# Optimization experiments

Hardware: AMD Instinct MI355X
Metric: run time of the kernel (lower is better)

Reference implementation:

```python
import jax, jax.numpy as jnp
import numpy as np

B, H, S, D = 4, 8, 2048, 64
NEG = -1e9


def setup_inputs() -> dict:
    key = jax.random.key(0)
    k1, k2, k3, k4 = jax.random.split(key, 4)
    qs = jax.random.normal(k1, (B, H, S, D), dtype=jnp.float32)
    ks = jax.random.normal(k2, (B, H, S, D), dtype=jnp.float32)
    vs = jax.random.normal(k3, (B, H, S, D), dtype=jnp.float32)
    # binary 0/1 float mask, broadcast over heads
    mask = (jax.random.uniform(k4, (B, 1, S, S)) < 0.5).astype(jnp.float32)
    return {"qs": qs, "ks": ks, "vs": vs, "mask": mask}


def reference(qs, ks, vs, mask):
    scale = 1.0 / np.sqrt(qs.shape[-1]).astype(np.float32)
    # [B,H,S,S] logits; multiplicative pre-mask, then additive -1e9 on masked slots
    logits = jnp.einsum('bhqd,bhkd->bhqk', qs, ks) * mask * scale
    logits = logits + (1.0 - mask) * NEG
    weights = jax.nn.softmax(logits, axis=-1) * mask  # multiplicative post-mask
    return jnp.einsum('bhqk,bhkd->bhqd', weights, vs)
```

## Files before the change

### kernel.cpp

```cpp
#include <hip/hip_runtime.h>
#include <stdint.h>

#define S_LEN 2048
#define NTILE 32

typedef float f32x4 __attribute__((ext_vector_type(4)));
typedef short bf16x8 __attribute__((ext_vector_type(8)));

__device__ __forceinline__ uint16_t f2bf(float f) {
    uint32_t u = __float_as_uint(f);
    return (uint16_t)((u + 0x7FFFu + ((u >> 16) & 1u)) >> 16);
}

#define SWZ(r, cb) (((r) << 7) + ((cb) ^ (((r) & 7) << 4)))

#define AS3PTR(p) ((__attribute__((address_space(3))) uint32_t*)(uintptr_t)(p))
#define AS1PTR(p) ((const __attribute__((address_space(1))) uint32_t*)(uintptr_t)(p))

__global__ __launch_bounds__(256)
void prep_all(const float* __restrict__ K, const float* __restrict__ V,
              const float* __restrict__ M, uint8_t* __restrict__ Kswz,
              uint8_t* __restrict__ Vtswz, unsigned long long* __restrict__ Mb)
{
    const int bid = blockIdx.x;
    const int tid = threadIdx.x;
    if (bid < 2048) {
        int flat = bid * 256 + tid;
        int cb = flat & 7, r = (flat >> 3) & 63, kt = (flat >> 9) & 31, bh = flat >> 14;
        const float* src = K + (((size_t)bh * S_LEN + kt * 64 + r) << 6) + cb * 8;
        f32x4 a = *(const f32x4*)src;
        f32x4 b = *(const f32x4*)(src + 4);
        bf16x8 o;
        o[0] = (short)f2bf(a[0]); o[1] = (short)f2bf(a[1]);
        o[2] = (short)f2bf(a[2]); o[3] = (short)f2bf(a[3]);
        o[4] = (short)f2bf(b[0]); o[5] = (short)f2bf(b[1]);
        o[6] = (short)f2bf(b[2]); o[7] = (short)f2bf(b[3]);
        *(bf16x8*)(Kswz + (((size_t)(bh * 32 + kt)) << 13) + SWZ(r, cb * 16)) = o;
    } else if (bid < 4096) {
        int flat = (bid - 2048) * 256 + tid;
        int d = flat & 63, ck = (flat >> 6) & 7, kt = (flat >> 9) & 31, bh = flat >> 14;
        const float* src = V + (((size_t)bh * S_LEN + kt * 64 + ck * 8) << 6) + d;
        bf16x8 o;
        #pragma unroll
        for (int i = 0; i < 8; ++i) o[i] = (short)f2bf(src[i << 6]);
        *(bf16x8*)(Vtswz + (((size_t)(bh * 32 + kt)) << 13) + SWZ(d, ck * 16)) = o;
    } else {
        int wave = (bid - 4096) * 4 + (tid >> 6);
        int lane = tid & 63;
        size_t w0 = (size_t)wave * 16;
        for (int i = 0; i < 16; ++i) {
            size_t widx = w0 + i;
            float m = M[(widx << 6) + lane];
            unsigned long long bits = __ballot(m > 0.5f);
            if (lane == 0) Mb[widx] = bits;
        }
    }
}

#define K_OFF 0
#define V_OFF 16384

__global__ __launch_bounds__(256, 4)
void attn_fwd(const float* __restrict__ Q, const uint8_t* __restrict__ Kswz,
              const uint8_t* __restrict__ Vtswz,
              const unsigned long long* __restrict__ Mb,
              float* __restrict__ O)
{
    __shared__ __align__(16) uint8_t lds[32768];

    const int tid  = threadIdx.x;
    const int lane = tid & 63;
    const int w    = tid >> 6;
    const int g    = lane >> 4;
    const int c    = lane & 15;

    const int bid0 = blockIdx.x;
    const int bid  = ((bid0 & 7) << 7) + (bid0 >> 3);
    const int bh  = bid >> 5;
    const int qt  = bid & 31;
    const int b   = bh >> 3;
    const int q0  = qt << 6;

    const float QSCL = 0.125f * 1.44269504088896340736f;
    bf16x8 qf[2];
    {
        const float* qrow = Q + (((size_t)bh * S_LEN + q0 + w * 16 + c) << 6);
        #pragma unroll
        for (int kb = 0; kb < 2; ++kb) {
            f32x4 a  = *(const f32x4*)(qrow + kb * 32 + g * 8);
            f32x4 b4 = *(const f32x4*)(qrow + kb * 32 + g * 8 + 4);
            bf16x8 f;
            f[0] = (short)f2bf(a[0] * QSCL);  f[1] = (short)f2bf(a[1] * QSCL);
            f[2] = (short)f2bf(a[2] * QSCL);  f[3] = (short)f2bf(a[3] * QSCL);
            f[4] = (short)f2bf(b4[0] * QSCL); f[5] = (short)f2bf(b4[1] * QSCL);
            f[6] = (short)f2bf(b4[2] * QSCL); f[7] = (short)f2bf(b4[3] * QSCL);
            qf[kb] = f;
        }
    }

    f32x4 acc[4];
    #pragma unroll
    for (int dt = 0; dt < 4; ++dt) acc[dt] = (f32x4){0.f, 0.f, 0.f, 0.f};
    float lsum = 0.f;

    const unsigned long long* mrow =
        Mb + ((size_t)(b * S_LEN + q0 + w * 16 + c) << 5);

    const uint8_t* kbh = Kswz  + ((size_t)(bh * 32) << 13);
    const uint8_t* vbh = Vtswz + ((size_t)(bh * 32) << 13);

    auto stage = [&](int buf, int t) {
        #pragma unroll
        for (int it = 0; it < 2; ++it) {
            int off = ((w << 1) + it) << 10;
            __builtin_amdgcn_global_load_lds(
                AS1PTR(kbh + ((size_t)t << 13) + off + lane * 16),
                AS3PTR(&lds[K_OFF + (buf << 13) + off]), 16, 0, 0);
            __builtin_amdgcn_global_load_lds(
                AS1PTR(vbh + ((size_t)t << 13) + off + lane * 16),
                AS3PTR(&lds[V_OFF + (buf << 13) + off]), 16, 0, 0);
        }
    };

    stage(0, 0);
    __syncthreads();

    #pragma unroll 2
    for (int kt = 0; kt < NTILE; ++kt) {
        const int buf = kt & 1;
        if (kt + 1 < NTILE) stage(buf ^ 1, kt + 1);

        unsigned long long mw = mrow[kt];

        const uint8_t* kb = &lds[K_OFF + (buf << 13)];
        f32x4 sacc[4];
        #pragma unroll
        for (int ct = 0; ct < 4; ++ct) {
            bf16x8 kf0 = *(const bf16x8*)(kb + SWZ(16 * ct + c, 16 * g));
            bf16x8 kf1 = *(const bf16x8*)(kb + SWZ(16 * ct + c, 64 + 16 * g));
            f32x4 z = (f32x4){0.f, 0.f, 0.f, 0.f};
            z = __builtin_amdgcn_mfma_f32_16x16x32_bf16(kf0, qf[0], z, 0, 0, 0);
            z = __builtin_amdgcn_mfma_f32_16x16x32_bf16(kf1, qf[1], z, 0, 0, 0);
            sacc[ct] = z;
        }

        uint32_t pd[4][2];
        unsigned long long msh = mw >> (4 * g);
        uint32_t ulo = (uint32_t)msh, uhi = (uint32_t)(msh >> 32);
        #pragma unroll
        for (int ct = 0; ct < 4; ++ct) {
            uint32_t sel = (ct & 2) ? uhi : ulo;
            float e[4];
            #pragma unroll
            for (int j = 0; j < 4; ++j) {
                float x = sacc[ct][j];
                x = (sel & (1u << (16 * (ct & 1) + j))) ? x : -1000.f;
                asm("v_exp_f32 %0, %1" : "=v"(e[j]) : "v"(x));
                lsum += e[j];
            }
            asm("v_cvt_pk_bf16_f32 %0, %1, %2" : "=v"(pd[ct][0]) : "v"(e[0]), "v"(e[1]));
            asm("v_cvt_pk_bf16_f32 %0, %1, %2" : "=v"(pd[ct][1]) : "v"(e[2]), "v"(e[3]));
        }

        const uint8_t* vb = &lds[V_OFF + (buf << 13)];
        #pragma unroll
        for (int kp = 0; kp < 2; ++kp) {
            uint32_t a0 = pd[2 * kp][0], b0 = pd[2 * kp + 1][0];
            uint32_t a1 = pd[2 * kp][1], b1 = pd[2 * kp + 1][1];
            asm("v_permlane32_swap_b32 %0, %1" : "+v"(a0), "+v"(b0));
            asm("v_permlane16_swap_b32 %0, %1" : "+v"(a0), "+v"(b0));
            asm("v_permlane32_swap_b32 %0, %1" : "+v"(a1), "+v"(b1));
            asm("v_permlane16_swap_b32 %0, %1" : "+v"(a1), "+v"(b1));
            union { uint32_t d[4]; bf16x8 v; } pu;
            pu.d[0] = a0; pu.d[1] = a1; pu.d[2] = b0; pu.d[3] = b1;
            #pragma unroll
            for (int dt = 0; dt < 4; ++dt) {
                bf16x8 vf = *(const bf16x8*)(vb + SWZ(c + 16 * dt, kp * 64 + 16 * g));
                acc[dt] = __builtin_amdgcn_mfma_f32_16x16x32_bf16(pu.v, vf, acc[dt], 0, 0, 0);
            }
        }

        __syncthreads();
    }

    float l = lsum;
    l += __shfl_xor(l, 16, 64);
    l += __shfl_xor(l, 32, 64);
    float linv = (l > 0.f) ? 1.f / l : 0.f;
    float inv[4];
    #pragma unroll
    for (int j = 0; j < 4; ++j) inv[j] = __shfl(linv, 4 * g + j, 64);

    float* obase = O + (((size_t)bh * S_LEN + q0 + w * 16) << 6);
    #pragma unroll
    for (int j = 0; j < 4; ++j)
        #pragma unroll
        for (int dt = 0; dt < 4; ++dt)
            obase[((4 * g + j) << 6) + c + 16 * dt] = acc[dt][j] * inv[j];
}

extern "C" void kernel_launch(void* const* d_in, const int* in_sizes, int n_in,
                              void* d_out, int out_size, void* d_ws, size_t ws_size,
                              hipStream_t stream) {
    const float* qs   = (const float*)d_in[0];
    const float* ks   = (const float*)d_in[1];
    const float* vs   = (const float*)d_in[2];
    const float* mask = (const float*)d_in[3];
    float* out = (float*)d_out;
    (void)in_sizes; (void)n_in; (void)out_size; (void)ws_size;

    uint8_t* ws = (uint8_t*)d_ws;
    uint8_t* Kswz  = ws;
    uint8_t* Vtswz = ws + (8u << 20);
    unsigned long long* Mb = (unsigned long long*)(ws + (16u << 20));

    hipLaunchKernelGGL(prep_all, dim3(8192), dim3(256), 0, stream,
                       ks, vs, mask, Kswz, Vtswz, Mb);
    hipLaunchKernelGGL(attn_fwd, dim3(1024), dim3(256), 0, stream,
                       qs, Kswz, Vtswz, Mb, out);
}
```

Baseline: 81.33 us.

## Split key tiles across waves with register-resident fragments and LDS reduction

Restructures attention so each wave handles all 64 query rows for a quarter of every key tile, loading K/V fragments straight from global memory into registers in MFMA-ready layouts instead of staging through shared memory with barriers. The prep kernel now writes K and V in per-lane fragment order and packs the mask into 16-bit words per lane via an LDS transpose. Partial outputs and row sums are combined across the four waves through LDS at the end. This removes per-tile barriers and LDS traffic, at the cost of more registers (occupancy hint lowered to 3), a cross-wave reduction, and a larger mask-prep phase.

```diff
diff --git a/kernel.cpp b/kernel.cpp
--- a/kernel.cpp
+++ b/kernel.cpp
@@ -6,22 +6,31 @@
 
 typedef float f32x4 __attribute__((ext_vector_type(4)));
 typedef short bf16x8 __attribute__((ext_vector_type(8)));
+typedef short s16x4 __attribute__((ext_vector_type(4)));
 
 __device__ __forceinline__ uint16_t f2bf(float f) {
     uint32_t u = __float_as_uint(f);
     return (uint16_t)((u + 0x7FFFu + ((u >> 16) & 1u)) >> 16);
 }
 
-#define SWZ(r, cb) (((r) << 7) + ((cb) ^ (((r) & 7) << 4)))
-
-#define AS3PTR(p) ((__attribute__((address_space(3))) uint32_t*)(uintptr_t)(p))
-#define AS1PTR(p) ((const __attribute__((address_space(1))) uint32_t*)(uintptr_t)(p))
+#if __has_builtin(__builtin_amdgcn_mfma_f32_16x16x16bf16_1k)
+__device__ __forceinline__ f32x4 mfma16(s16x4 a, s16x4 b, f32x4 c) {
+    return __builtin_amdgcn_mfma_f32_16x16x16bf16_1k(a, b, c, 0, 0, 0);
+}
+#else
+__device__ __forceinline__ f32x4 mfma16(s16x4 a, s16x4 b, f32x4 c) {
+    bf16x8 az = {a[0], a[1], a[2], a[3], 0, 0, 0, 0};
+    bf16x8 bz = {b[0], b[1], b[2], b[3], 0, 0, 0, 0};
+    return __builtin_amdgcn_mfma_f32_16x16x32_bf16(az, bz, c, 0, 0, 0);
+}
+#endif
 
 __global__ __launch_bounds__(256)
 void prep_all(const float* __restrict__ K, const float* __restrict__ V,
-              const float* __restrict__ M, uint8_t* __restrict__ Kswz,
-              uint8_t* __restrict__ Vtswz, unsigned long long* __restrict__ Mb)
+              const float* __restrict__ M, uint8_t* __restrict__ Kd,
+              uint8_t* __restrict__ Vd, uint16_t* __restrict__ Mp)
 {
+    __shared__ float mt[4096];
     const int bid = blockIdx.x;
     const int tid = threadIdx.x;
     if (bid < 2048) {
@@ -35,38 +44,48 @@
         o[2] = (short)f2bf(a[2]); o[3] = (short)f2bf(a[3]);
         o[4] = (short)f2bf(b[0]); o[5] = (short)f2bf(b[1]);
         o[6] = (short)f2bf(b[2]); o[7] = (short)f2bf(b[3]);
-        *(bf16x8*)(Kswz + (((size_t)(bh * 32 + kt)) << 13) + SWZ(r, cb * 16)) = o;
-    } else if (bid < 4096) {
-        int flat = (bid - 2048) * 256 + tid;
-        int d = flat & 63, ck = (flat >> 6) & 7, kt = (flat >> 9) & 31, bh = flat >> 14;
-        const float* src = V + (((size_t)bh * S_LEN + kt * 64 + ck * 8) << 6) + d;
-        bf16x8 o;
-        #pragma unroll
-        for (int i = 0; i < 8; ++i) o[i] = (short)f2bf(src[i << 6]);
-        *(bf16x8*)(Vtswz + (((size_t)(bh * 32 + kt)) << 13) + SWZ(d, ck * 16)) = o;
+        size_t chunk = ((((size_t)(bh * 32 + kt) * 4 + (r >> 4)) * 2 + (cb >> 2)) << 6)
+                       + ((cb & 3) << 4) + (r & 15);
+        *(bf16x8*)(Kd + chunk * 16) = o;
+    } else if (bid < 6144) {
+        int vf = (bid - 2048) * 256 + tid;
+        int c = vf & 15, g = (vf >> 4) & 3, dt = (vf >> 6) & 3;
+        int w = (vf >> 8) & 3, kt = (vf >> 10) & 31, bh = vf >> 15;
+        const float* src = V + (((size_t)bh * S_LEN + kt * 64 + 16 * w + 4 * g) << 6)
+                           + 16 * dt + c;
+        s16x4 o;
+        #pragma unroll
+        for (int j = 0; j < 4; ++j) o[j] = (short)f2bf(src[j << 6]);
+        size_t chunk = (((size_t)(bh * 32 + kt) * 16 + w * 4 + dt) << 6) + g * 16 + c;
+        *(s16x4*)(Vd + chunk * 8) = o;
     } else {
-        int wave = (bid - 4096) * 4 + (tid >> 6);
-        int lane = tid & 63;
-        size_t w0 = (size_t)wave * 16;
-        for (int i = 0; i < 16; ++i) {
-            size_t widx = w0 + i;
-            float m = M[(widx << 6) + lane];
-            unsigned long long bits = __ballot(m > 0.5f);
-            if (lane == 0) Mb[widx] = bits;
-        }
-    }
-}
-
-#define K_OFF 0
-#define V_OFF 16384
-
-__global__ __launch_bounds__(256, 4)
-void attn_fwd(const float* __restrict__ Q, const uint8_t* __restrict__ Kswz,
-              const uint8_t* __restrict__ Vtswz,
-              const unsigned long long* __restrict__ Mb,
+        int mid = bid - 6144;
+        int b = mid >> 10, qt = (mid >> 5) & 31, kt = mid & 31;
+        int row = tid >> 2, cc = tid & 3;
+        const float* src = M + ((size_t)(b * S_LEN + qt * 64 + row) * S_LEN) + kt * 64;
+        #pragma unroll
+        for (int i = 0; i < 4; ++i)
+            *(f32x4*)&mt[(row << 6) + cc * 16 + i * 4] =
+                *(const f32x4*)(src + cc * 16 + i * 4);
+        __syncthreads();
+        int l = tid & 63, w = tid >> 6, g = l >> 4, c = l & 15;
+        uint32_t m = 0;
+        #pragma unroll
+        for (int qc = 0; qc < 4; ++qc)
+            #pragma unroll
+            for (int j = 0; j < 4; ++j)
+                m |= (mt[((16 * qc + c) << 6) + 16 * w + 4 * g + j] > 0.5f)
+                     << (qc * 4 + j);
+        Mp[(size_t)mid * 256 + tid] = (uint16_t)m;
+    }
+}
+
+__global__ __launch_bounds__(256, 3)
+void attn_fwd(const float* __restrict__ Q, const uint8_t* __restrict__ Kd,
+              const uint8_t* __restrict__ Vd, const uint16_t* __restrict__ Mp,
               float* __restrict__ O)
 {
-    __shared__ __align__(16) uint8_t lds[32768];
+    __shared__ __align__(16) uint8_t lds[33792];
 
     const int tid  = threadIdx.x;
     const int lane = tid & 63;
@@ -82,121 +101,137 @@
     const int q0  = qt << 6;
 
     const float QSCL = 0.125f * 1.44269504088896340736f;
-    bf16x8 qf[2];
-    {
-        const float* qrow = Q + (((size_t)bh * S_LEN + q0 + w * 16 + c) << 6);
-        #pragma unroll
-        for (int kb = 0; kb < 2; ++kb) {
-            f32x4 a  = *(const f32x4*)(qrow + kb * 32 + g * 8);
-            f32x4 b4 = *(const f32x4*)(qrow + kb * 32 + g * 8 + 4);
+    bf16x8 qf[4][2];
+    #pragma unroll
+    for (int qc = 0; qc < 4; ++qc) {
+        const float* qrow = Q + (((size_t)bh * S_LEN + q0 + 16 * qc + c) << 6);
+        #pragma unroll
+        for (int dk = 0; dk < 2; ++dk) {
+            f32x4 a  = *(const f32x4*)(qrow + dk * 32 + g * 8);
+            f32x4 b4 = *(const f32x4*)(qrow + dk * 32 + g * 8 + 4);
             bf16x8 f;
             f[0] = (short)f2bf(a[0] * QSCL);  f[1] = (short)f2bf(a[1] * QSCL);
             f[2] = (short)f2bf(a[2] * QSCL);  f[3] = (short)f2bf(a[3] * QSCL);
             f[4] = (short)f2bf(b4[0] * QSCL); f[5] = (short)f2bf(b4[1] * QSCL);
             f[6] = (short)f2bf(b4[2] * QSCL); f[7] = (short)f2bf(b4[3] * QSCL);
-            qf[kb] = f;
+            qf[qc][dk] = f;
         }
     }
 
-    f32x4 acc[4];
-    #pragma unroll
-    for (int dt = 0; dt < 4; ++dt) acc[dt] = (f32x4){0.f, 0.f, 0.f, 0.f};
-    float lsum = 0.f;
-
-    const unsigned long long* mrow =
-        Mb + ((size_t)(b * S_LEN + q0 + w * 16 + c) << 5);
-
-    const uint8_t* kbh = Kswz  + ((size_t)(bh * 32) << 13);
-    const uint8_t* vbh = Vtswz + ((size_t)(bh * 32) << 13);
-
-    auto stage = [&](int buf, int t) {
-        #pragma unroll
-        for (int it = 0; it < 2; ++it) {
-            int off = ((w << 1) + it) << 10;
-            __builtin_amdgcn_global_load_lds(
-                AS1PTR(kbh + ((size_t)t << 13) + off + lane * 16),
-                AS3PTR(&lds[K_OFF + (buf << 13) + off]), 16, 0, 0);
-            __builtin_amdgcn_global_load_lds(
-                AS1PTR(vbh + ((size_t)t << 13) + off + lane * 16),
-                AS3PTR(&lds[V_OFF + (buf << 13) + off]), 16, 0, 0);
-        }
-    };
-
-    stage(0, 0);
-    __syncthreads();
-
-    #pragma unroll 2
-    for (int kt = 0; kt < NTILE; ++kt) {
-        const int buf = kt & 1;
-        if (kt + 1 < NTILE) stage(buf ^ 1, kt + 1);
-
-        unsigned long long mw = mrow[kt];
-
-        const uint8_t* kb = &lds[K_OFF + (buf << 13)];
-        f32x4 sacc[4];
-        #pragma unroll
-        for (int ct = 0; ct < 4; ++ct) {
-            bf16x8 kf0 = *(const bf16x8*)(kb + SWZ(16 * ct + c, 16 * g));
-            bf16x8 kf1 = *(const bf16x8*)(kb + SWZ(16 * ct + c, 64 + 16 * g));
-            f32x4 z = (f32x4){0.f, 0.f, 0.f, 0.f};
-            z = __builtin_amdgcn_mfma_f32_16x16x32_bf16(kf0, qf[0], z, 0, 0, 0);
-            z = __builtin_amdgcn_mfma_f32_16x16x32_bf16(kf1, qf[1], z, 0, 0, 0);
-            sacc[ct] = z;
-        }
-
-        uint32_t pd[4][2];
-        unsigned long long msh = mw >> (4 * g);
-        uint32_t ulo = (uint32_t)msh, uhi = (uint32_t)(msh >> 32);
-        #pragma unroll
-        for (int ct = 0; ct < 4; ++ct) {
-            uint32_t sel = (ct & 2) ? uhi : ulo;
-            float e[4];
-            #pragma unroll
-            for (int j = 0; j < 4; ++j) {
-                float x = sacc[ct][j];
-                x = (sel & (1u << (16 * (ct & 1) + j))) ? x : -1000.f;
-                asm("v_exp_f32 %0, %1" : "=v"(e[j]) : "v"(x));
-                lsum += e[j];
-            }
-            asm("v_cvt_pk_bf16_f32 %0, %1, %2" : "=v"(pd[ct][0]) : "v"(e[0]), "v"(e[1]));
-            asm("v_cvt_pk_bf16_f32 %0, %1, %2" : "=v"(pd[ct][1]) : "v"(e[2]), "v"(e[3]));
-        }
-
-        const uint8_t* vb = &lds[V_OFF + (buf << 13)];
-        #pragma unroll
-        for (int kp = 0; kp < 2; ++kp) {
-            uint32_t a0 = pd[2 * kp][0], b0 = pd[2 * kp + 1][0];
-            uint32_t a1 = pd[2 * kp][1], b1 = pd[2 * kp + 1][1];
-            asm("v_permlane32_swap_b32 %0, %1" : "+v"(a0), "+v"(b0));
-            asm("v_permlane16_swap_b32 %0, %1" : "+v"(a0), "+v"(b0));
-            asm("v_permlane32_swap_b32 %0, %1" : "+v"(a1), "+v"(b1));
-            asm("v_permlane16_swap_b32 %0, %1" : "+v"(a1), "+v"(b1));
-            union { uint32_t d[4]; bf16x8 v; } pu;
-            pu.d[0] = a0; pu.d[1] = a1; pu.d[2] = b0; pu.d[3] = b1;
-            #pragma unroll
-            for (int dt = 0; dt < 4; ++dt) {
-                bf16x8 vf = *(const bf16x8*)(vb + SWZ(c + 16 * dt, kp * 64 + 16 * g));
-                acc[dt] = __builtin_amdgcn_mfma_f32_16x16x32_bf16(pu.v, vf, acc[dt], 0, 0, 0);
-            }
-        }
-
-        __syncthreads();
-    }
-
-    float l = lsum;
-    l += __shfl_xor(l, 16, 64);
-    l += __shfl_xor(l, 32, 64);
-    float linv = (l > 0.f) ? 1.f / l : 0.f;
-    float inv[4];
-    #pragma unroll
-    for (int j = 0; j < 4; ++j) inv[j] = __shfl(linv, 4 * g + j, 64);
-
-    float* obase = O + (((size_t)bh * S_LEN + q0 + w * 16) << 6);
-    #pragma unroll
-    for (int j = 0; j < 4; ++j)
-        #pragma unroll
-        for (int dt = 0; dt < 4; ++dt)
-            obase[((4 * g + j) << 6) + c + 16 * dt] = acc[dt][j] * inv[j];
+    f32x4 acc[4][4];
+    #pragma unroll
+    for (int qc = 0; qc < 4; ++qc)
+        #pragma unroll
+        for (int dt = 0; dt < 4; ++dt) acc[qc][dt] = (f32x4){0.f, 0.f, 0.f, 0.f};
+    float lsum[4] = {0.f, 0.f, 0.f, 0.f};
+
+    const uint8_t*  kbase = Kd + (((size_t)bh * 32) << 13) + ((w << 1) << 10) + (lane << 4);
+    const uint8_t*  vbase = Vd + (((size_t)bh * 32) << 13) + ((w << 2) << 9) + (lane << 3);
+    const uint16_t* mbase = Mp + (((size_t)(b * 32 + qt) * 32) << 8) + (w << 6) + lane;
+
+    bf16x8 ka[2][2];
+    s16x4  vb[2][4];
+    uint32_t mw[2];
+
+#define LOADT(BUF, T)                                                          \
+    {                                                                          \
+        ka[BUF][0] = *(const bf16x8*)(kbase + ((size_t)(T) << 13));            \
+        ka[BUF][1] = *(const bf16x8*)(kbase + ((size_t)(T) << 13) + 1024);     \
+        _Pragma("unroll")                                                      \
+        for (int dt = 0; dt < 4; ++dt)                                         \
+            vb[BUF][dt] = *(const s16x4*)(vbase + ((size_t)(T) << 13) + (dt << 9)); \
+        mw[BUF] = mbase[(size_t)(T) << 8];                                     \
+    }
+
+#define COMPUTE(BUF)                                                           \
+    {                                                                          \
+        f32x4 sacc[4];                                                         \
+        _Pragma("unroll")                                                      \
+        for (int qc = 0; qc < 4; ++qc) {                                       \
+            f32x4 z = (f32x4){0.f, 0.f, 0.f, 0.f};                             \
+            z = __builtin_amdgcn_mfma_f32_16x16x32_bf16(ka[BUF][0], qf[qc][0], z, 0, 0, 0); \
+            z = __builtin_amdgcn_mfma_f32_16x16x32_bf16(ka[BUF][1], qf[qc][1], z, 0, 0, 0); \
+            sacc[qc] = z;                                                      \
+        }                                                                      \
+        _Pragma("unroll")                                                      \
+        for (int qc = 0; qc < 4; ++qc) {                                       \
+            float e[4];                                                        \
+            _Pragma("unroll")                                                  \
+            for (int j = 0; j < 4; ++j) {                                      \
+                float x = (mw[BUF] & (1u << (qc * 4 + j))) ? sacc[qc][j] : -1000.f; \
+                asm("v_exp_f32 %0, %1" : "=v"(e[j]) : "v"(x));                 \
+                lsum[qc] += e[j];                                              \
+            }                                                                  \
+            union { uint32_t d[2]; s16x4 v; } pu;                              \
+            asm("v_cvt_pk_bf16_f32 %0, %1, %2" : "=v"(pu.d[0]) : "v"(e[0]), "v"(e[1])); \
+            asm("v_cvt_pk_bf16_f32 %0, %1, %2" : "=v"(pu.d[1]) : "v"(e[2]), "v"(e[3])); \
+            _Pragma("unroll")                                                  \
+            for (int dt = 0; dt < 4; ++dt)                                     \
+                acc[qc][dt] = mfma16(pu.v, vb[BUF][dt], acc[qc][dt]);          \
+        }                                                                      \
+    }
+
+    LOADT(0, 0);
+    #pragma unroll 1
+    for (int kt = 0; kt < NTILE; kt += 2) {
+        LOADT(1, kt + 1);
+        COMPUTE(0);
+        if (kt + 2 < NTILE) LOADT(0, kt + 2);
+        COMPUTE(1);
+    }
+
+    float* A  = (float*)lds;
+    float* Bu = (float*)(lds + 16384);
+    float* LS = (float*)(lds + 32768);
+
+    #pragma unroll
+    for (int qc = 0; qc < 4; ++qc) {
+        lsum[qc] += __shfl_xor(lsum[qc], 16, 64);
+        lsum[qc] += __shfl_xor(lsum[qc], 32, 64);
+    }
+    if (g == 0) {
+        #pragma unroll
+        for (int qc = 0; qc < 4; ++qc) LS[(w << 6) + (qc << 4) + c] = lsum[qc];
+    }
+
+#define WRACC(R)                                                               \
+    { _Pragma("unroll")                                                        \
+      for (int qc = 0; qc < 4; ++qc) _Pragma("unroll")                         \
+      for (int dt = 0; dt < 4; ++dt)                                           \
+          *(f32x4*)((R) + ((((qc << 2) + dt) << 6) + lane) * 4) = acc[qc][dt]; }
+#define RDADD(R)                                                               \
+    { _Pragma("unroll")                                                        \
+      for (int qc = 0; qc < 4; ++qc) _Pragma("unroll")                         \
+      for (int dt = 0; dt < 4; ++dt)                                           \
+          acc[qc][dt] += *(const f32x4*)((R) + ((((qc << 2) + dt) << 6) + lane) * 4); }
+
+    if (w == 1) WRACC(A);
+    if (w == 3) WRACC(Bu);
+    __syncthreads();
+    if (w == 0) RDADD(A);
+    if (w == 2) RDADD(Bu);
+    __syncthreads();
+    if (w == 2) WRACC(A);
+    __syncthreads();
+    if (w == 0) { RDADD(A); WRACC(Bu); }
+    __syncthreads();
+
+    float lt[4];
+    #pragma unroll
+    for (int j = 0; j < 4; ++j) {
+        float s = 0.f;
+        #pragma unroll
+        for (int wp = 0; wp < 4; ++wp) s += LS[(wp << 6) + (w << 4) + 4 * g + j];
+        lt[j] = (s > 0.f) ? 1.f / s : 0.f;
+    }
+    float* obase = O + (((size_t)bh * S_LEN + q0 + (w << 4)) << 6);
+    #pragma unroll
+    for (int dt = 0; dt < 4; ++dt) {
+        f32x4 v = *(const f32x4*)(Bu + ((((w << 2) + dt) << 6) + lane) * 4);
+        #pragma unroll
+        for (int j = 0; j < 4; ++j)
+            obase[((4 * g + j) << 6) + c + 16 * dt] = v[j] * lt[j];
+    }
 }
 
 extern "C" void kernel_launch(void* const* d_in, const int* in_sizes, int n_in,
@@ -210,12 +245,12 @@
     (void)in_sizes; (void)n_in; (void)out_size; (void)ws_size;
 
     uint8_t* ws = (uint8_t*)d_ws;
-    uint8_t* Kswz  = ws;
-    uint8_t* Vtswz = ws + (8u << 20);
-    unsigned long long* Mb = (unsigned long long*)(ws + (16u << 20));
-
-    hipLaunchKernelGGL(prep_all, dim3(8192), dim3(256), 0, stream,
-                       ks, vs, mask, Kswz, Vtswz, Mb);
+    uint8_t* Kd = ws;
+    uint8_t* Vd = ws + (8u << 20);
+    uint16_t* Mp = (uint16_t*)(ws + (16u << 20));
+
+    hipLaunchKernelGGL(prep_all, dim3(10240), dim3(256), 0, stream,
+                       ks, vs, mask, Kd, Vd, Mp);
     hipLaunchKernelGGL(attn_fwd, dim3(1024), dim3(256), 0, stream,
-                       qs, Kswz, Vtswz, Mb, out);
-}
+                       qs, Kd, Vd, Mp, out);
+}
```

After: 78.70 us. 3.2% less time.

## Switch attention to 32x32x16 MFMA with split-key waves and per-lane mask packing

Applied to the files above, without the earlier changes.

Moves the attention kernel from 16x16x32 to 32x32x16 bf16 MFMA tiles. Each block now has two query waves and two key-half waves, and the two key halves are reduced through LDS at the end. K/V are pre-laid out in a fragment-major format, so the XOR swizzle is no longer needed. The mask is pre-packed into 16-bit per-lane words via an LDS transpose in the prep kernel. The aim is fewer MFMA issues and permlane shuffles per tile. In exchange it adds a final cross-wave reduction, a heavier mask-prep stage with shared memory, and possible LDS bank conflicts from the unswizzled layout.

```diff
diff --git a/kernel.cpp b/kernel.cpp
--- a/kernel.cpp
+++ b/kernel.cpp
@@ -5,6 +5,7 @@
 #define NTILE 32
 
 typedef float f32x4 __attribute__((ext_vector_type(4)));
+typedef float f32x16 __attribute__((ext_vector_type(16)));
 typedef short bf16x8 __attribute__((ext_vector_type(8)));
 
 __device__ __forceinline__ uint16_t f2bf(float f) {
@@ -12,22 +13,23 @@
     return (uint16_t)((u + 0x7FFFu + ((u >> 16) & 1u)) >> 16);
 }
 
-#define SWZ(r, cb) (((r) << 7) + ((cb) ^ (((r) & 7) << 4)))
-
 #define AS3PTR(p) ((__attribute__((address_space(3))) uint32_t*)(uintptr_t)(p))
 #define AS1PTR(p) ((const __attribute__((address_space(1))) uint32_t*)(uintptr_t)(p))
 
 __global__ __launch_bounds__(256)
 void prep_all(const float* __restrict__ K, const float* __restrict__ V,
-              const float* __restrict__ M, uint8_t* __restrict__ Kswz,
-              uint8_t* __restrict__ Vtswz, unsigned long long* __restrict__ Mb)
+              const float* __restrict__ M, uint8_t* __restrict__ Kd,
+              uint8_t* __restrict__ Vd, uint16_t* __restrict__ Mp)
 {
+    __shared__ float mt[4096];
     const int bid = blockIdx.x;
     const int tid = threadIdx.x;
     if (bid < 2048) {
         int flat = bid * 256 + tid;
-        int cb = flat & 7, r = (flat >> 3) & 63, kt = (flat >> 9) & 31, bh = flat >> 14;
-        const float* src = K + (((size_t)bh * S_LEN + kt * 64 + r) << 6) + cb * 8;
+        int s = flat & 511, tile = flat >> 9;
+        int key = s >> 3, dc = (s >> 1) & 3, h = s & 1;
+        int kt = tile & 31, bh = tile >> 5;
+        const float* src = K + (((size_t)bh * S_LEN + kt * 64 + key) << 6) + dc * 16 + h * 8;
         f32x4 a = *(const f32x4*)src;
         f32x4 b = *(const f32x4*)(src + 4);
         bf16x8 o;
@@ -35,25 +37,36 @@
         o[2] = (short)f2bf(a[2]); o[3] = (short)f2bf(a[3]);
         o[4] = (short)f2bf(b[0]); o[5] = (short)f2bf(b[1]);
         o[6] = (short)f2bf(b[2]); o[7] = (short)f2bf(b[3]);
-        *(bf16x8*)(Kswz + (((size_t)(bh * 32 + kt)) << 13) + SWZ(r, cb * 16)) = o;
+        *(bf16x8*)(Kd + ((size_t)tile << 13) + (((dc * 2 + h) * 64 + key) << 4)) = o;
     } else if (bid < 4096) {
         int flat = (bid - 2048) * 256 + tid;
-        int d = flat & 63, ck = (flat >> 6) & 7, kt = (flat >> 9) & 31, bh = flat >> 14;
-        const float* src = V + (((size_t)bh * S_LEN + kt * 64 + ck * 8) << 6) + d;
+        int s = flat & 511, tile = flat >> 9;
+        int d = s & 63, h = (s >> 6) & 1, ku = s >> 7;
+        int kt = tile & 31, bh = tile >> 5;
+        const float* src = V + (((size_t)bh * S_LEN + kt * 64 + ku * 16 + h * 8) << 6) + d;
         bf16x8 o;
         #pragma unroll
-        for (int i = 0; i < 8; ++i) o[i] = (short)f2bf(src[i << 6]);
-        *(bf16x8*)(Vtswz + (((size_t)(bh * 32 + kt)) << 13) + SWZ(d, ck * 16)) = o;
+        for (int j = 0; j < 8; ++j) o[j] = (short)f2bf(src[j << 6]);
+        *(bf16x8*)(Vd + ((size_t)tile << 13) + (((ku * 2 + h) * 64 + d) << 4)) = o;
     } else {
-        int wave = (bid - 4096) * 4 + (tid >> 6);
-        int lane = tid & 63;
-        size_t w0 = (size_t)wave * 16;
-        for (int i = 0; i < 16; ++i) {
-            size_t widx = w0 + i;
-            float m = M[(widx << 6) + lane];
-            unsigned long long bits = __ballot(m > 0.5f);
-            if (lane == 0) Mb[widx] = bits;
-        }
+        int mid = bid - 4096;
+        int b = mid >> 10, qt = (mid >> 5) & 31, kt = mid & 31;
+        int row = tid >> 2, cc = tid & 3;
+        const float* src = M + ((size_t)(b * S_LEN + qt * 64 + row) * S_LEN) + kt * 64;
+        #pragma unroll
+        for (int i = 0; i < 4; ++i)
+            *(f32x4*)&mt[(row << 6) + cc * 16 + i * 4] =
+                *(const f32x4*)(src + cc * 16 + i * 4);
+        __syncthreads();
+        int l = tid & 63, w = tid >> 6;
+        int qw = w >> 1, kw = w & 1, h = l >> 5, l31 = l & 31;
+        uint32_t m = 0;
+        #pragma unroll
+        for (int r = 0; r < 16; ++r) {
+            int keyl = 32 * kw + (r & 3) + 8 * (r >> 2) + 4 * h;
+            m |= (mt[((32 * qw + l31) << 6) + keyl] > 0.5f) << r;
+        }
+        Mp[((size_t)mid << 8) + tid] = (uint16_t)m;
     }
 }
 
@@ -61,9 +74,8 @@
 #define V_OFF 16384
 
 __global__ __launch_bounds__(256, 4)
-void attn_fwd(const float* __restrict__ Q, const uint8_t* __restrict__ Kswz,
-              const uint8_t* __restrict__ Vtswz,
-              const unsigned long long* __restrict__ Mb,
+void attn_fwd(const float* __restrict__ Q, const uint8_t* __restrict__ Kd,
+              const uint8_t* __restrict__ Vd, const uint16_t* __restrict__ Mp,
               float* __restrict__ O)
 {
     __shared__ __align__(16) uint8_t lds[32768];
@@ -71,8 +83,10 @@
     const int tid  = threadIdx.x;
     const int lane = tid & 63;
     const int w    = tid >> 6;
-    const int g    = lane >> 4;
-    const int c    = lane & 15;
+    const int qw   = w >> 1;
+    const int kw   = w & 1;
+    const int h    = lane >> 5;
+    const int l31  = lane & 31;
 
     const int bid0 = blockIdx.x;
     const int bid  = ((bid0 & 7) << 7) + (bid0 >> 3);
@@ -82,42 +96,40 @@
     const int q0  = qt << 6;
 
     const float QSCL = 0.125f * 1.44269504088896340736f;
-    bf16x8 qf[2];
+    bf16x8 qf[4];
     {
-        const float* qrow = Q + (((size_t)bh * S_LEN + q0 + w * 16 + c) << 6);
-        #pragma unroll
-        for (int kb = 0; kb < 2; ++kb) {
-            f32x4 a  = *(const f32x4*)(qrow + kb * 32 + g * 8);
-            f32x4 b4 = *(const f32x4*)(qrow + kb * 32 + g * 8 + 4);
+        const float* qrow = Q + (((size_t)bh * S_LEN + q0 + 32 * qw + l31) << 6);
+        #pragma unroll
+        for (int dc = 0; dc < 4; ++dc) {
+            f32x4 a  = *(const f32x4*)(qrow + dc * 16 + h * 8);
+            f32x4 b4 = *(const f32x4*)(qrow + dc * 16 + h * 8 + 4);
             bf16x8 f;
             f[0] = (short)f2bf(a[0] * QSCL);  f[1] = (short)f2bf(a[1] * QSCL);
             f[2] = (short)f2bf(a[2] * QSCL);  f[3] = (short)f2bf(a[3] * QSCL);
             f[4] = (short)f2bf(b4[0] * QSCL); f[5] = (short)f2bf(b4[1] * QSCL);
             f[6] = (short)f2bf(b4[2] * QSCL); f[7] = (short)f2bf(b4[3] * QSCL);
-            qf[kb] = f;
-        }
-    }
-
-    f32x4 acc[4];
-    #pragma unroll
-    for (int dt = 0; dt < 4; ++dt) acc[dt] = (f32x4){0.f, 0.f, 0.f, 0.f};
+            qf[dc] = f;
+        }
+    }
+
+    f32x16 acc[2];
+    acc[0] = (f32x16)(0.f);
+    acc[1] = (f32x16)(0.f);
     float lsum = 0.f;
 
-    const unsigned long long* mrow =
-        Mb + ((size_t)(b * S_LEN + q0 + w * 16 + c) << 5);
-
-    const uint8_t* kbh = Kswz  + ((size_t)(bh * 32) << 13);
-    const uint8_t* vbh = Vtswz + ((size_t)(bh * 32) << 13);
+    const uint8_t*  ktb = Kd + (((size_t)bh * 32) << 13);
+    const uint8_t*  vtb = Vd + (((size_t)bh * 32) << 13);
+    const uint16_t* mbase = Mp + (((size_t)(b * 32 + qt) * 32) << 8) + (w << 6) + lane;
 
     auto stage = [&](int buf, int t) {
         #pragma unroll
-        for (int it = 0; it < 2; ++it) {
-            int off = ((w << 1) + it) << 10;
+        for (int i = 0; i < 2; ++i) {
+            int off = (i << 12) + (w << 10);
             __builtin_amdgcn_global_load_lds(
-                AS1PTR(kbh + ((size_t)t << 13) + off + lane * 16),
+                AS1PTR(ktb + ((size_t)t << 13) + off + lane * 16),
                 AS3PTR(&lds[K_OFF + (buf << 13) + off]), 16, 0, 0);
             __builtin_amdgcn_global_load_lds(
-                AS1PTR(vbh + ((size_t)t << 13) + off + lane * 16),
+                AS1PTR(vtb + ((size_t)t << 13) + off + lane * 16),
                 AS3PTR(&lds[V_OFF + (buf << 13) + off]), 16, 0, 0);
         }
     };
@@ -130,73 +142,90 @@
         const int buf = kt & 1;
         if (kt + 1 < NTILE) stage(buf ^ 1, kt + 1);
 
-        unsigned long long mw = mrow[kt];
+        uint32_t mw = mbase[kt << 8];
 
         const uint8_t* kb = &lds[K_OFF + (buf << 13)];
-        f32x4 sacc[4];
-        #pragma unroll
-        for (int ct = 0; ct < 4; ++ct) {
-            bf16x8 kf0 = *(const bf16x8*)(kb + SWZ(16 * ct + c, 16 * g));
-            bf16x8 kf1 = *(const bf16x8*)(kb + SWZ(16 * ct + c, 64 + 16 * g));
-            f32x4 z = (f32x4){0.f, 0.f, 0.f, 0.f};
-            z = __builtin_amdgcn_mfma_f32_16x16x32_bf16(kf0, qf[0], z, 0, 0, 0);
-            z = __builtin_amdgcn_mfma_f32_16x16x32_bf16(kf1, qf[1], z, 0, 0, 0);
-            sacc[ct] = z;
-        }
-
-        uint32_t pd[4][2];
-        unsigned long long msh = mw >> (4 * g);
-        uint32_t ulo = (uint32_t)msh, uhi = (uint32_t)(msh >> 32);
-        #pragma unroll
-        for (int ct = 0; ct < 4; ++ct) {
-            uint32_t sel = (ct & 2) ? uhi : ulo;
-            float e[4];
+        f32x16 s = (f32x16)(0.f);
+        #pragma unroll
+        for (int dc = 0; dc < 4; ++dc) {
+            bf16x8 kf = *(const bf16x8*)(kb + (((dc * 2 + h) * 64 + 32 * kw + l31) << 4));
+            s = __builtin_amdgcn_mfma_f32_32x32x16_bf16(kf, qf[dc], s, 0, 0, 0);
+        }
+
+        uint32_t pd[8];
+        #pragma unroll
+        for (int rq = 0; rq < 8; ++rq) {
+            float x0 = (mw & (1u << (2 * rq)))     ? s[2 * rq]     : -1000.f;
+            float x1 = (mw & (1u << (2 * rq + 1))) ? s[2 * rq + 1] : -1000.f;
+            float e0, e1;
+            asm("v_exp_f32 %0, %1" : "=v"(e0) : "v"(x0));
+            asm("v_exp_f32 %0, %1" : "=v"(e1) : "v"(x1));
+            lsum += e0 + e1;
+            asm("v_cvt_pk_bf16_f32 %0, %1, %2" : "=v"(pd[rq]) : "v"(e0), "v"(e1));
+        }
+
+        #pragma unroll
+        for (int u = 0; u < 2; ++u) {
+            asm("v_permlane32_swap_b32 %0, %1" : "+v"(pd[4 * u]),     "+v"(pd[4 * u + 2]));
+            asm("v_permlane32_swap_b32 %0, %1" : "+v"(pd[4 * u + 1]), "+v"(pd[4 * u + 3]));
+        }
+
+        const uint8_t* vbuf = &lds[V_OFF + (buf << 13)];
+        #pragma unroll
+        for (int u = 0; u < 2; ++u) {
+            union { uint32_t d[4]; bf16x8 v; } pa;
+            pa.d[0] = pd[4 * u]; pa.d[1] = pd[4 * u + 1];
+            pa.d[2] = pd[4 * u + 2]; pa.d[3] = pd[4 * u + 3];
             #pragma unroll
-            for (int j = 0; j < 4; ++j) {
-                float x = sacc[ct][j];
-                x = (sel & (1u << (16 * (ct & 1) + j))) ? x : -1000.f;
-                asm("v_exp_f32 %0, %1" : "=v"(e[j]) : "v"(x));
-                lsum += e[j];
+            for (int dblk = 0; dblk < 2; ++dblk) {
+                bf16x8 vf = *(const bf16x8*)(vbuf +
+                    ((((kw * 2 + u) * 2 + h) * 64 + 32 * dblk + l31) << 4));
+                acc[dblk] = __builtin_amdgcn_mfma_f32_32x32x16_bf16(pa.v, vf, acc[dblk], 0, 0, 0);
             }
-            asm("v_cvt_pk_bf16_f32 %0, %1, %2" : "=v"(pd[ct][0]) : "v"(e[0]), "v"(e[1]));
-            asm("v_cvt_pk_bf16_f32 %0, %1, %2" : "=v"(pd[ct][1]) : "v"(e[2]), "v"(e[3]));
-        }
-
-        const uint8_t* vb = &lds[V_OFF + (buf << 13)];
-        #pragma unroll
-        for (int kp = 0; kp < 2; ++kp) {
-            uint32_t a0 = pd[2 * kp][0], b0 = pd[2 * kp + 1][0];
-            uint32_t a1 = pd[2 * kp][1], b1 = pd[2 * kp + 1][1];
-            asm("v_permlane32_swap_b32 %0, %1" : "+v"(a0), "+v"(b0));
-            asm("v_permlane16_swap_b32 %0, %1" : "+v"(a0), "+v"(b0));
-            asm("v_permlane32_swap_b32 %0, %1" : "+v"(a1), "+v"(b1));
-            asm("v_permlane16_swap_b32 %0, %1" : "+v"(a1), "+v"(b1));
-            union { uint32_t d[4]; bf16x8 v; } pu;
-            pu.d[0] = a0; pu.d[1] = a1; pu.d[2] = b0; pu.d[3] = b1;
+        }
+
+        __syncthreads();
+    }
+
+    lsum += __shfl_xor(lsum, 32, 64);
+
+    float* ex  = (float*)lds;
+    float* ex2 = (float*)(lds + 16384);
+    if (kw == 1) {
+        #pragma unroll
+        for (int dblk = 0; dblk < 2; ++dblk)
             #pragma unroll
-            for (int dt = 0; dt < 4; ++dt) {
-                bf16x8 vf = *(const bf16x8*)(vb + SWZ(c + 16 * dt, kp * 64 + 16 * g));
-                acc[dt] = __builtin_amdgcn_mfma_f32_16x16x32_bf16(pu.v, vf, acc[dt], 0, 0, 0);
+            for (int rq = 0; rq < 4; ++rq) {
+                f32x4 v = { acc[dblk][4 * rq], acc[dblk][4 * rq + 1],
+                            acc[dblk][4 * rq + 2], acc[dblk][4 * rq + 3] };
+                *(f32x4*)&ex[(qw << 11) + (((dblk << 2) + rq) << 8) + (lane << 2)] = v;
             }
-        }
-
-        __syncthreads();
-    }
-
-    float l = lsum;
-    l += __shfl_xor(l, 16, 64);
-    l += __shfl_xor(l, 32, 64);
-    float linv = (l > 0.f) ? 1.f / l : 0.f;
-    float inv[4];
-    #pragma unroll
-    for (int j = 0; j < 4; ++j) inv[j] = __shfl(linv, 4 * g + j, 64);
-
-    float* obase = O + (((size_t)bh * S_LEN + q0 + w * 16) << 6);
-    #pragma unroll
-    for (int j = 0; j < 4; ++j)
-        #pragma unroll
-        for (int dt = 0; dt < 4; ++dt)
-            obase[((4 * g + j) << 6) + c + 16 * dt] = acc[dt][j] * inv[j];
+        if (lane < 32) ex2[(qw << 5) + lane] = lsum;
+    }
+    __syncthreads();
+    if (kw == 0) {
+        #pragma unroll
+        for (int dblk = 0; dblk < 2; ++dblk)
+            #pragma unroll
+            for (int rq = 0; rq < 4; ++rq) {
+                f32x4 v = *(const f32x4*)&ex[(qw << 11) + (((dblk << 2) + rq) << 8) + (lane << 2)];
+                acc[dblk][4 * rq]     += v[0];
+                acc[dblk][4 * rq + 1] += v[1];
+                acc[dblk][4 * rq + 2] += v[2];
+                acc[dblk][4 * rq + 3] += v[3];
+            }
+        float l = lsum + ex2[(qw << 5) + l31];
+        float linv = (l > 0.f) ? 1.f / l : 0.f;
+
+        float* obase = O + (((size_t)bh * S_LEN + q0 + 32 * qw) << 6);
+        #pragma unroll
+        for (int r = 0; r < 16; ++r) {
+            int qloc = (r & 3) + 8 * (r >> 2) + 4 * h;
+            float inv = __shfl(linv, qloc, 64);
+            obase[(qloc << 6) + l31]      = acc[0][r] * inv;
+            obase[(qloc << 6) + 32 + l31] = acc[1][r] * inv;
+        }
+    }
 }
 
 extern "C" void kernel_launch(void* const* d_in, const int* in_sizes, int n_in,
@@ -210,12 +239,12 @@
     (void)in_sizes; (void)n_in; (void)out_size; (void)ws_size;
 
     uint8_t* ws = (uint8_t*)d_ws;
-    uint8_t* Kswz  = ws;
-    uint8_t* Vtswz = ws + (8u << 20);
-    unsigned long long* Mb = (unsigned long long*)(ws + (16u << 20));
+    uint8_t* Kd = ws;
+    uint8_t* Vd = ws + (8u << 20);
+    uint16_t* Mp = (uint16_t*)(ws + (16u << 20));
 
     hipLaunchKernelGGL(prep_all, dim3(8192), dim3(256), 0, stream,
-                       ks, vs, mask, Kswz, Vtswz, Mb);
+                       ks, vs, mask, Kd, Vd, Mp);
     hipLaunchKernelGGL(attn_fwd, dim3(1024), dim3(256), 0, stream,
-                       qs, Kswz, Vtswz, Mb, out);
-}
+                       qs, Kd, Vd, Mp, out);
+}
```

Measured after the change: 79.29 us. 2.5% less time.
